# Kernel optimization log

Hardware: AMD Instinct MI355X
Metric: run time of the kernel (lower is better)

Reference implementation:

```python
import jax, jax.numpy as jnp
import numpy as np

H = 1024   # hidden_size
NH = 16    # num heads
DH = H // NH
L = 2      # attention levels
E = 8      # experts
F = 4 * H  # expert FFN hidden
B = 2
S = 1024
EPS = 1e-5
TOPK = 2
STD = 0.02


def setup_inputs() -> dict:
    key = jax.random.key(0)
    ks = jax.random.split(key, 12)
    def n(k, shp):
        return jax.random.normal(k, shp, jnp.float32) * STD
    return {
        "hidden_states": jax.random.normal(ks[0], (B, S, H), jnp.float32),
        "attention_mask": jnp.ones((B, S), jnp.int32),
        "ln1_g": jnp.ones((H,), jnp.float32), "ln1_b": jnp.zeros((H,), jnp.float32),
        "ln2_g": jnp.ones((H,), jnp.float32), "ln2_b": jnp.zeros((H,), jnp.float32),
        "Wq": n(ks[1], (L, H, H)), "Wk": n(ks[2], (L, H, H)),
        "Wv": n(ks[3], (L, H, H)), "Wo": n(ks[4], (L, H, H)),
        "bq": jnp.zeros((L, H), jnp.float32), "bk": jnp.zeros((L, H), jnp.float32),
        "bv": jnp.zeros((L, H), jnp.float32), "bo": jnp.zeros((L, H), jnp.float32),
        "level_logits": n(ks[5], (L,)),
        "Wr": n(ks[6], (H, E)), "br": jnp.zeros((E,), jnp.float32),
        "W1": n(ks[7], (E, H, F)), "b1": jnp.zeros((E, F), jnp.float32),
        "W2": n(ks[8], (E, F, H)), "b2": jnp.zeros((E, H), jnp.float32),
    }


def _ln(x, g, b):
    m = x.mean(-1, keepdims=True)
    v = x.var(-1, keepdims=True)
    return (x - m) * jax.lax.rsqrt(v + EPS) * g + b


def _mla(x, mask_f, Wq, Wk, Wv, Wo, bq, bk, bv, bo, level_logits):
    # Multi-level attention: one MHA per level, softmax-combined over levels.
    b_, s_, _ = x.shape
    def proj(W, bias):
        y = jnp.einsum('bsh,lhd->lbsd', x, W) + bias[:, None, None, :]
        return y.reshape(L, b_, s_, NH, DH)
    q, k, v = proj(Wq, bq), proj(Wk, bk), proj(Wv, bv)
    scores = jnp.einsum('lbqnd,lbknd->lbnqk', q, k) / np.float32(np.sqrt(DH))
    bias = (1.0 - mask_f)[None, :, None, None, :] * jnp.float32(-1e9)  # key-side mask
    attn = jax.nn.softmax(scores + bias, axis=-1)
    ctx = jnp.einsum('lbnqk,lbknd->lbqnd', attn, v).reshape(L, b_, s_, H)
    out = jnp.einsum('lbsh,lhd->lbsd', ctx, Wo) + bo[:, None, None, :]
    w = jax.nn.softmax(level_logits)
    return jnp.einsum('l,lbsd->bsd', w, out)


def _moe(x, Wr, br, W1, b1, W2, b2):
    # Top-2 softmax router with renormalized gates; dense expert compute,
    # sparse combine (math-equivalent to dispatch/combine without dropping).
    logits = x @ Wr + br                                  # [B,S,E]
    probs = jax.nn.softmax(logits, axis=-1)
    topv, topi = jax.lax.top_k(probs, TOPK)               # [B,S,K]
    gates = topv / topv.sum(-1, keepdims=True)
    combine = jnp.sum(jax.nn.one_hot(topi, E, dtype=x.dtype) * gates[..., None], axis=-2)  # [B,S,E]
    h = jax.nn.gelu(jnp.einsum('bsh,ehf->besf', x, W1) + b1[None, :, None, :])
    y = jnp.einsum('besf,efh->besh', h, W2) + b2[None, :, None, :]
    return jnp.einsum('bse,besh->bsh', combine, y), logits


def reference(hidden_states, attention_mask, ln1_g, ln1_b, ln2_g, ln2_b,
              Wq, Wk, Wv, Wo, bq, bk, bv, bo, level_logits,
              Wr, br, W1, b1, W2, b2):
    mask_f = attention_mask.astype(jnp.float32)
    attn = _mla(_ln(hidden_states, ln1_g, ln1_b), mask_f,
                Wq, Wk, Wv, Wo, bq, bk, bv, bo, level_logits)
    x = hidden_states + attn                  # residual 1 (dropout in eval = identity)
    moe_out, _router_logits = _moe(_ln(x, ln2_g, ln2_b), Wr, br, W1, b1, W2, b2)
    return x + moe_out                        # residual 2
```

## Files before the change

kernel.cpp:

```cpp
#include <hip/hip_runtime.h>
#include <hip/hip_bf16.h>
#include <stdint.h>

#define Hn   1024
#define NHn  16
#define DHn  64
#define Ln   2
#define En   8
#define Fn   4096
#define Bn   2
#define Sn   1024
#define Tn   2048
#define An   4096
#define KSPLIT 4

typedef __bf16 bf16_t;
typedef __bf16 bf16x2 __attribute__((ext_vector_type(2)));
typedef __bf16 bf16x4 __attribute__((ext_vector_type(4)));
typedef __bf16 bf16x8 __attribute__((ext_vector_type(8)));
typedef float  f32x4  __attribute__((ext_vector_type(4)));

__device__ __forceinline__ f32x4 mfma16(bf16x8 a, bf16x8 b, f32x4 c){
  return __builtin_amdgcn_mfma_f32_16x16x32_bf16(a, b, c, 0, 0, 0);
}
__device__ __forceinline__ void gload16(const void* gsrc, void* ldst){
  __builtin_amdgcn_global_load_lds((const __attribute__((address_space(1))) void*)gsrc,
                                   (__attribute__((address_space(3))) void*)ldst, 16, 0, 0);
}
__device__ __forceinline__ float gelu_f(float x){
  float u = 0.7978845608028654f * (x + 0.044715f * x * x * x);
  return 0.5f * x * (1.0f + tanhf(u));
}

__global__ __launch_bounds__(256)
void tcvt_k(const float* __restrict__ src, bf16_t* __restrict__ dst, int R, int C){
  __shared__ float tile[32][33];
  size_t moff = (size_t)blockIdx.z * R * C;
  src += moff; dst += moff;
  int c0 = blockIdx.x * 32, r0 = blockIdx.y * 32;
  int tx = threadIdx.x & 31, ty = threadIdx.x >> 5;
  #pragma unroll
  for (int i = 0; i < 32; i += 8)
    tile[ty + i][tx] = src[(size_t)(r0 + ty + i) * C + (c0 + tx)];
  __syncthreads();
  #pragma unroll
  for (int i = 0; i < 32; i += 8)
    dst[(size_t)(c0 + ty + i) * R + (r0 + tx)] = (bf16_t)tile[tx][ty + i];
}

__global__ __launch_bounds__(256)
void ln_k(const float* __restrict__ x, const float* __restrict__ gam,
          const float* __restrict__ bet, bf16_t* __restrict__ out){
  int row = blockIdx.x;
  const float4* xr = (const float4*)(x + (size_t)row * Hn);
  int t = threadIdx.x, lane = t & 63, w = t >> 6;
  float4 v = xr[t];
  float s  = v.x + v.y + v.z + v.w;
  float ss = v.x*v.x + v.y*v.y + v.z*v.z + v.w*v.w;
  #pragma unroll
  for (int mk = 1; mk < 64; mk <<= 1){ s += __shfl_xor(s, mk); ss += __shfl_xor(ss, mk); }
  __shared__ float r1[4], r2[4];
  if (lane == 0){ r1[w] = s; r2[w] = ss; }
  __syncthreads();
  float S1 = r1[0]+r1[1]+r1[2]+r1[3];
  float S2 = r2[0]+r2[1]+r2[2]+r2[3];
  float mean = S1 * (1.0f/Hn);
  float var  = S2 * (1.0f/Hn) - mean*mean;
  float rstd = rsqrtf(var + 1e-5f);
  int c = t * 4;
  bf16_t* o = out + (size_t)row * Hn + c;
  o[0] = (bf16_t)((v.x-mean)*rstd*gam[c+0] + bet[c+0]);
  o[1] = (bf16_t)((v.y-mean)*rstd*gam[c+1] + bet[c+1]);
  o[2] = (bf16_t)((v.z-mean)*rstd*gam[c+2] + bet[c+2]);
  o[3] = (bf16_t)((v.w-mean)*rstd*gam[c+3] + bet[c+3]);
}

__global__ __launch_bounds__(256)
void res_ln2_k(const float* __restrict__ x, const float* __restrict__ o0,
               const float* __restrict__ o1, const float* __restrict__ lvl,
               const float* __restrict__ gam, const float* __restrict__ bet,
               float* __restrict__ x2, bf16_t* __restrict__ xn2){
  int row = blockIdx.x, t = threadIdx.x, lane = t & 63, w = t >> 6;
  float l0 = lvl[0], l1 = lvl[1];
  float mx = fmaxf(l0, l1);
  float e0 = __expf(l0 - mx), e1 = __expf(l1 - mx);
  float inv = 1.f / (e0 + e1);
  float w0 = e0 * inv, w1 = e1 * inv;
  size_t base = (size_t)row * Hn;
  float4 xv = ((const float4*)(x  + base))[t];
  float4 a0 = ((const float4*)(o0 + base))[t];
  float4 a1 = ((const float4*)(o1 + base))[t];
  float4 v;
  v.x = xv.x + w0*a0.x + w1*a1.x;
  v.y = xv.y + w0*a0.y + w1*a1.y;
  v.z = xv.z + w0*a0.z + w1*a1.z;
  v.w = xv.w + w0*a0.w + w1*a1.w;
  ((float4*)(x2 + base))[t] = v;
  float s  = v.x + v.y + v.z + v.w;
  float ss = v.x*v.x + v.y*v.y + v.z*v.z + v.w*v.w;
  #pragma unroll
  for (int mk = 1; mk < 64; mk <<= 1){ s += __shfl_xor(s, mk); ss += __shfl_xor(ss, mk); }
  __shared__ float r1[4], r2[4];
  if (lane == 0){ r1[w] = s; r2[w] = ss; }
  __syncthreads();
  float S1 = r1[0]+r1[1]+r1[2]+r1[3];
  float S2 = r2[0]+r2[1]+r2[2]+r2[3];
  float mean = S1 * (1.0f/Hn);
  float var  = S2 * (1.0f/Hn) - mean*mean;
  float rstd = rsqrtf(var + 1e-5f);
  int c = t * 4;
  bf16_t* o = xn2 + base + c;
  o[0] = (bf16_t)((v.x-mean)*rstd*gam[c+0] + bet[c+0]);
  o[1] = (bf16_t)((v.y-mean)*rstd*gam[c+1] + bet[c+1]);
  o[2] = (bf16_t)((v.z-mean)*rstd*gam[c+2] + bet[c+2]);
  o[3] = (bf16_t)((v.w-mean)*rstd*gam[c+3] + bet[c+3]);
}

struct GP {
  const bf16_t* A;
  const bf16_t* Bt;
  const float*  bias;
  float*        fout;
  bf16_t*       bfout;
  const int*    list;
  const int*    counts;
  int Kstride;
  int Kloc;
};

template<int MODE>
__global__ __launch_bounds__(256)
void gemm_k(GP p){
  const int nt = blockIdx.x, mt = blockIdx.y, z = blockIdx.z;
  const bf16_t* A = p.A;
  const bf16_t* Bt = p.Bt;
  const float* bias = p.bias;
  const int* list = nullptr;
  int cnt = 0x7fffffff;
  int kbase = 0;
  if constexpr (MODE == 0){
    Bt += (size_t)z*Hn*Hn; bias += z*Hn;
  } else if constexpr (MODE == 1){
    Bt += (size_t)z*Hn*Hn; bias += z*Hn; A += (size_t)z*Bn*Sn*Hn;
  } else if constexpr (MODE == 3){
    cnt = p.counts[z];
    if (mt * 128 >= cnt) return;
    list = p.list + z * Tn;
    Bt += (size_t)z*Fn*Hn; bias += z*Fn;
  } else {
    int e = z >> 2;
    cnt = p.counts[e];
    if (mt * 128 >= cnt) return;
    list = p.list + e * Tn;
    Bt += (size_t)e*Hn*Fn; bias += e*Hn;
    kbase = (z & 3) * (Fn / KSPLIT);
  }
  const int Ks = p.Kstride;
  const int NT = p.Kloc >> 5;

  __shared__ bf16_t As[2][128*32];
  __shared__ bf16_t Bs[2][128*32];
  const int tid = threadIdx.x, lane = tid & 63, w = tid >> 6;
  const int wr = (w >> 1) * 64, wc = (w & 1) * 64;
  const int lane15 = lane & 15, kg = lane >> 4;

  const bf16_t* aptr[2];
  const bf16_t* bptr[2];
  int chunks[2];
  #pragma unroll
  for (int i = 0; i < 2; ++i){
    int ch = w*64 + lane + i*256;
    chunks[i] = ch;
    int row = ch >> 2, kc = (ch & 3) * 8;
    int ar;
    if constexpr (MODE == 3){ int g = mt*128 + row; if (g >= cnt) g = cnt - 1; ar = list[g] >> 1; }
    else if constexpr (MODE == 4){ int g = mt*128 + row; if (g >= cnt) g = cnt - 1; ar = list[g]; }
    else ar = mt*128 + row;
    aptr[i] = A  + (size_t)ar * Ks + kbase + kc;
    bptr[i] = Bt + (size_t)(nt*128 + row) * Ks + kbase + kc;
  }

  const f32x4 fz = {0.f,0.f,0.f,0.f};
  f32x4 acc[4][4];
  #pragma unroll
  for (int m = 0; m < 4; ++m)
    #pragma unroll
    for (int n = 0; n < 4; ++n) acc[m][n] = fz;

  #pragma unroll
  for (int i = 0; i < 2; ++i){
    gload16(aptr[i], &As[0][chunks[i]*8]);
    gload16(bptr[i], &Bs[0][chunks[i]*8]);
  }
  __syncthreads();

  int cur = 0;
  for (int t = 0; t < NT; ++t){
    if (t + 1 < NT){
      int k1 = (t+1) * 32;
      #pragma unroll
      for (int i = 0; i < 2; ++i){
        gload16(aptr[i] + k1, &As[cur^1][chunks[i]*8]);
        gload16(bptr[i] + k1, &Bs[cur^1][chunks[i]*8]);
      }
    }
    bf16x8 af[4], bfr[4];
    #pragma unroll
    for (int m = 0; m < 4; ++m) af[m]  = *(const bf16x8*)(&As[cur][(wr + m*16 + lane15)*32 + kg*8]);
    #pragma unroll
    for (int n = 0; n < 4; ++n) bfr[n] = *(const bf16x8*)(&Bs[cur][(wc + n*16 + lane15)*32 + kg*8]);
    #pragma unroll
    for (int m = 0; m < 4; ++m)
      #pragma unroll
      for (int n = 0; n < 4; ++n)
        acc[m][n] = mfma16(af[m], bfr[n], acc[m][n]);
    __syncthreads();
    cur ^= 1;
  }

  if constexpr (MODE == 0){
    bf16_t* outp = p.bfout + (size_t)z * (Bn*NHn*Sn*DHn);
    if (z < 4){
      #pragma unroll
      for (int m = 0; m < 4; ++m){
        int row0 = mt*128 + wr + m*16 + kg*4;
        #pragma unroll
        for (int n = 0; n < 4; ++n){
          int col = nt*128 + wc + n*16 + lane15;
          int nh = col >> 6, dh = col & 63;
          float bv = bias[col];
          f32x4 v = acc[m][n];
          #pragma unroll
          for (int r = 0; r < 4; ++r){
            int tk = row0 + r;
            int bb = tk >> 10, s = tk & 1023;
            outp[((size_t)(bb*NHn + nh)*Sn + s)*DHn + dh] = (bf16_t)(v[r] + bv);
          }
        }
      }
    } else {
      #pragma unroll
      for (int m = 0; m < 4; ++m){
        int row0 = mt*128 + wr + m*16 + kg*4;
        int bb = row0 >> 10, s = row0 & 1023;
        #pragma unroll
        for (int n = 0; n < 4; ++n){
          int col = nt*128 + wc + n*16 + lane15;
          int nh = col >> 6, dh = col & 63;
          float bv = bias[col];
          f32x4 v = acc[m][n];
          bf16x4 pk;
          pk[0] = (bf16_t)(v[0] + bv);
          pk[1] = (bf16_t)(v[1] + bv);
          pk[2] = (bf16_t)(v[2] + bv);
          pk[3] = (bf16_t)(v[3] + bv);
          *(bf16x4*)(outp + ((size_t)(bb*NHn + nh)*DHn + dh)*Sn + s) = pk;
        }
      }
    }
  } else if constexpr (MODE == 1){
    float* outp = p.fout + (size_t)z * Tn * Hn;
    #pragma unroll
    for (int m = 0; m < 4; ++m){
      int row0 = mt*128 + wr + m*16 + kg*4;
      #pragma unroll
      for (int n = 0; n < 4; ++n){
        int col = nt*128 + wc + n*16 + lane15;
        float bv = bias[col];
        f32x4 v = acc[m][n];
        #pragma unroll
        for (int r = 0; r < 4; ++r)
          outp[(size_t)(row0 + r)*Hn + col] = v[r] + bv;
      }
    }
  } else if constexpr (MODE == 3){
    #pragma unroll
    for (int m = 0; m < 4; ++m){
      int row0 = mt*128 + wr + m*16 + kg*4;
      #pragma unroll
      for (int n = 0; n < 4; ++n){
        int col = nt*128 + wc + n*16 + lane15;
        float bv = bias[col];
        f32x4 v = acc[m][n];
        #pragma unroll
        for (int r = 0; r < 4; ++r){
          int g = row0 + r;
          if (g < cnt){
            int aid = list[g];
            p.bfout[(size_t)aid*Fn + col] = (bf16_t)gelu_f(v[r] + bv);
          }
        }
      }
    }
  } else {
    float* outp = p.fout + (size_t)(z & 3) * An * Hn;
    bool addb = (z & 3) == 0;
    #pragma unroll
    for (int m = 0; m < 4; ++m){
      int row0 = mt*128 + wr + m*16 + kg*4;
      #pragma unroll
      for (int n = 0; n < 4; ++n){
        int col = nt*128 + wc + n*16 + lane15;
        float bv = addb ? bias[col] : 0.f;
        f32x4 v = acc[m][n];
        #pragma unroll
        for (int r = 0; r < 4; ++r){
          int g = row0 + r;
          if (g < cnt){
            int aid = list[g];
            outp[(size_t)aid*Hn + col] = v[r] + bv;
          }
        }
      }
    }
  }
}

__global__ __launch_bounds__(256)
void attn_k(const bf16_t* __restrict__ qh, const bf16_t* __restrict__ kh,
            const bf16_t* __restrict__ vtb, const int* __restrict__ amask,
            bf16_t* __restrict__ ctxb){
  int z  = blockIdx.x;
  int qb = blockIdx.y;
  int lvl = z >> 5, bb = (z >> 4) & 1, nh = z & 15;
  int tid = threadIdx.x, lane = tid & 63, w = tid >> 6;
  int lane15 = lane & 15, kg = lane >> 4;
  const bf16_t* Q  = qh  + (size_t)z * Sn * DHn;
  const bf16_t* Kp = kh  + (size_t)z * Sn * DHn;
  const bf16_t* Vt = vtb + (size_t)z * DHn * Sn;
  const int* mrow = amask + bb * Sn;
  __shared__ bf16_t Ks[2][32*64];
  __shared__ bf16_t Vs[2][64*32];
  __shared__ float bias_lds[Sn];
  __shared__ bf16_t p_lds[4][16*40];
  {
    int4 mv = ((const int4*)mrow)[tid];
    float4 bv;
    bv.x = mv.x ? 0.f : -1e9f;
    bv.y = mv.y ? 0.f : -1e9f;
    bv.z = mv.z ? 0.f : -1e9f;
    bv.w = mv.w ? 0.f : -1e9f;
    ((float4*)bias_lds)[tid] = bv;
  }
  int krow = w*8 + (lane >> 3);
  const bf16_t* ksrc = Kp + (size_t)krow*DHn + (((lane&7) ^ (krow&7)) << 3);
  int vrow = w*16 + (lane >> 2);
  const bf16_t* vsrc = Vt + (size_t)vrow*Sn + ((((lane&3) ^ ((vrow>>2)&3))) << 3);
  bf16_t* kdst[2] = { &Ks[0][w*512 + lane*8], &Ks[1][w*512 + lane*8] };
  bf16_t* vdst[2] = { &Vs[0][w*512 + lane*8], &Vs[1][w*512 + lane*8] };

  const f32x4 fz = {0.f,0.f,0.f,0.f};
  int qt = qb*4 + w;
  int qr = qt*16 + lane15;
  bf16x8 qa0 = *(const bf16x8*)(Q + (size_t)qr*DHn + kg*8);
  bf16x8 qa1 = *(const bf16x8*)(Q + (size_t)qr*DHn + 32 + kg*8);
  f32x4 ctxa[4] = {fz, fz, fz, fz};
  float m_ln = -1e30f;
  float s_ln = 0.f;
  float m_out[4] = {-1e30f,-1e30f,-1e30f,-1e30f};

  const int kslot0 = (kg ^ (lane15 & 7));
  const int kslot1 = ((kg + 4) ^ (lane15 & 7));
  const int ka_off0 = lane15*64 + kslot0*8;
  const int ka_off1 = lane15*64 + kslot1*8;
  const int kb_off0 = (16 + lane15)*64 + kslot0*8;
  const int kb_off1 = (16 + lane15)*64 + kslot1*8;

  gload16(ksrc, kdst[0]);
  gload16(vsrc, vdst[0]);
  __syncthreads();

  for (int kc = 0; kc < 32; ++kc){
    const int cur = kc & 1;
    const bf16_t* Kb = Ks[cur];
    const bf16_t* Vb = Vs[cur];
    if (kc + 1 < 32){
      gload16(ksrc + (size_t)(kc+1)*32*DHn, kdst[cur^1]);
      gload16(vsrc + (kc+1)*32,             vdst[cur^1]);
    }
    int k0 = kc * 32;
    bf16x8 ka0 = *(const bf16x8*)(Kb + ka_off0);
    bf16x8 ka1 = *(const bf16x8*)(Kb + ka_off1);
    bf16x8 kb0 = *(const bf16x8*)(Kb + kb_off0);
    bf16x8 kb1 = *(const bf16x8*)(Kb + kb_off1);
    f32x4 sA = mfma16(ka1, qa1, mfma16(ka0, qa0, fz));
    f32x4 sB = mfma16(kb1, qa1, mfma16(kb0, qa0, fz));
    float4 biasA = *(const float4*)(bias_lds + k0 + kg*4);
    float4 biasB = *(const float4*)(bias_lds + k0 + 16 + kg*4);
    float sv[8];
    sv[0] = sA[0]*0.125f + biasA.x;
    sv[1] = sA[1]*0.125f + biasA.y;
    sv[2] = sA[2]*0.125f + biasA.z;
    sv[3] = sA[3]*0.125f + biasA.w;
    sv[4] = sB[0]*0.125f + biasB.x;
    sv[5] = sB[1]*0.125f + biasB.y;
    sv[6] = sB[2]*0.125f + biasB.z;
    sv[7] = sB[3]*0.125f + biasB.w;
    float mx = fmaxf(fmaxf(fmaxf(sv[0],sv[1]),fmaxf(sv[2],sv[3])),
                     fmaxf(fmaxf(sv[4],sv[5]),fmaxf(sv[6],sv[7])));
    mx = fmaxf(mx, __shfl_xor(mx, 16));
    mx = fmaxf(mx, __shfl_xor(mx, 32));
    if (!__all(mx <= m_ln)){
      float mnew = fmaxf(m_ln, mx);
      s_ln *= __expf(m_ln - mnew);
      #pragma unroll
      for (int r = 0; r < 4; ++r){
        float mo = __shfl(mnew, kg*4 + r);
        float corr = __expf(m_out[r] - mo);
        ctxa[0][r] *= corr; ctxa[1][r] *= corr; ctxa[2][r] *= corr; ctxa[3][r] *= corr;
        m_out[r] = mo;
      }
      m_ln = mnew;
    }
    float pv[8];
    #pragma unroll
    for (int j = 0; j < 8; ++j){ pv[j] = __expf(sv[j] - m_ln); s_ln += pv[j]; }
    bf16_t* pr = p_lds[w] + lane15*40;
    *(bf16x2*)(pr + kg*4)          = (bf16x2){(bf16_t)pv[0], (bf16_t)pv[1]};
    *(bf16x2*)(pr + kg*4 + 2)      = (bf16x2){(bf16_t)pv[2], (bf16_t)pv[3]};
    *(bf16x2*)(pr + 16 + kg*4)     = (bf16x2){(bf16_t)pv[4], (bf16_t)pv[5]};
    *(bf16x2*)(pr + 16 + kg*4 + 2) = (bf16x2){(bf16_t)pv[6], (bf16_t)pv[7]};
    bf16x8 paf = *(const bf16x8*)(p_lds[w] + lane15*40 + kg*8);
    #pragma unroll
    for (int df = 0; df < 4; ++df){
      int r = df*16 + lane15;
      bf16x8 vbf = *(const bf16x8*)(Vb + r*32 + ((kg ^ ((r>>2)&3)) << 3));
      ctxa[df] = mfma16(paf, vbf, ctxa[df]);
    }
    __syncthreads();
  }
  s_ln += __shfl_xor(s_ln, 16);
  s_ln += __shfl_xor(s_ln, 32);
  #pragma unroll
  for (int r = 0; r < 4; ++r){
    float inv = 1.f / __shfl(s_ln, kg*4 + r);
    int srow = qt*16 + kg*4 + r;
    #pragma unroll
    for (int df = 0; df < 4; ++df){
      int d = df*16 + lane15;
      ctxb[((size_t)(lvl*2 + bb)*Sn + srow)*Hn + nh*DHn + d] = (bf16_t)(ctxa[df][r] * inv);
    }
  }
}

__global__ __launch_bounds__(64)
void router_k(const float* __restrict__ x2, const float* __restrict__ gam,
              const float* __restrict__ bet, const float* __restrict__ Wr,
              const float* __restrict__ br, float* __restrict__ gates,
              int* __restrict__ lists, int* __restrict__ counts){
  int t = blockIdx.x, lane = threadIdx.x;
  const float4* xr = (const float4*)(x2 + (size_t)t * Hn);
  float4 vbuf[4];
  float s = 0.f, ss = 0.f;
  #pragma unroll
  for (int i = 0; i < 4; ++i){
    float4 v = xr[lane + i*64];
    vbuf[i] = v;
    s  += v.x + v.y + v.z + v.w;
    ss += v.x*v.x + v.y*v.y + v.z*v.z + v.w*v.w;
  }
  #pragma unroll
  for (int mk = 1; mk < 64; mk <<= 1){ s += __shfl_xor(s, mk); ss += __shfl_xor(ss, mk); }
  float mean = s * (1.0f/Hn);
  float var  = ss * (1.0f/Hn) - mean*mean;
  float rstd = rsqrtf(var + 1e-5f);
  float a[8] = {0,0,0,0,0,0,0,0};
  #pragma unroll
  for (int i = 0; i < 4; ++i){
    int c = (lane + i*64) * 4;
    float4 v = vbuf[i];
    float xn[4] = {
      (v.x-mean)*rstd*gam[c+0] + bet[c+0],
      (v.y-mean)*rstd*gam[c+1] + bet[c+1],
      (v.z-mean)*rstd*gam[c+2] + bet[c+2],
      (v.w-mean)*rstd*gam[c+3] + bet[c+3]};
    #pragma unroll
    for (int j = 0; j < 4; ++j){
      const float* w = Wr + (size_t)(c + j) * En;
      #pragma unroll
      for (int e8 = 0; e8 < 8; ++e8) a[e8] += xn[j] * w[e8];
    }
  }
  #pragma unroll
  for (int e8 = 0; e8 < 8; ++e8)
    #pragma unroll
    for (int mk = 1; mk < 64; mk <<= 1) a[e8] += __shfl_xor(a[e8], mk);
  if (lane == 0){
    float lg[8]; float mx = -1e30f;
    #pragma unroll
    for (int e8 = 0; e8 < 8; ++e8){ lg[e8] = a[e8] + br[e8]; mx = fmaxf(mx, lg[e8]); }
    float p[8];
    #pragma unroll
    for (int e8 = 0; e8 < 8; ++e8) p[e8] = __expf(lg[e8] - mx);
    int i0 = 0; float v0 = p[0];
    #pragma unroll
    for (int e8 = 1; e8 < 8; ++e8) if (p[e8] > v0){ v0 = p[e8]; i0 = e8; }
    int i1 = -1; float v1 = -1.f;
    #pragma unroll
    for (int e8 = 0; e8 < 8; ++e8) if (e8 != i0 && p[e8] > v1){ v1 = p[e8]; i1 = e8; }
    float g0 = v0 / (v0 + v1), g1 = v1 / (v0 + v1);
    gates[2*t] = g0; gates[2*t+1] = g1;
    int s0 = atomicAdd(&counts[i0], 1); lists[i0*Tn + s0] = 2*t;
    int s1 = atomicAdd(&counts[i1], 1); lists[i1*Tn + s1] = 2*t + 1;
  }
}

__global__ __launch_bounds__(256)
void comb_k(const float* __restrict__ x2, const float* __restrict__ P,
            const float* __restrict__ gates, float* __restrict__ out){
  int t = blockIdx.x, i = threadIdx.x;
  float g0 = gates[2*t], g1 = gates[2*t+1];
  const size_t PS = (size_t)An * Hn;
  f32x4 s0 = {0,0,0,0}, s1 = {0,0,0,0};
  #pragma unroll
  for (int ks = 0; ks < KSPLIT; ++ks){
    f32x4 u0 = ((const f32x4*)(P + ks*PS + (size_t)(2*t)*Hn))[i];
    f32x4 u1 = ((const f32x4*)(P + ks*PS + (size_t)(2*t+1)*Hn))[i];
    s0 += u0; s1 += u1;
  }
  f32x4 va = ((const f32x4*)(x2 + (size_t)t*Hn))[i];
  f32x4 o = va + g0*s0 + g1*s1;
  ((f32x4*)(out + (size_t)t*Hn))[i] = o;
}

extern "C" void kernel_launch(void* const* d_in, const int* in_sizes, int n_in,
                              void* d_out, int out_size, void* d_ws, size_t ws_size,
                              hipStream_t stream)
{
  const float* x    = (const float*)d_in[0];
  const int* amask  = (const int*)d_in[1];
  const float* ln1g = (const float*)d_in[2];
  const float* ln1b = (const float*)d_in[3];
  const float* ln2g = (const float*)d_in[4];
  const float* ln2b = (const float*)d_in[5];
  const float* Wq   = (const float*)d_in[6];
  const float* Wk   = (const float*)d_in[7];
  const float* Wv   = (const float*)d_in[8];
  const float* Wo   = (const float*)d_in[9];
  const float* bq   = (const float*)d_in[10];
  const float* bk   = (const float*)d_in[11];
  const float* bv   = (const float*)d_in[12];
  const float* bo   = (const float*)d_in[13];
  const float* lvl  = (const float*)d_in[14];
  const float* Wr   = (const float*)d_in[15];
  const float* br   = (const float*)d_in[16];
  const float* W1   = (const float*)d_in[17];
  const float* b1   = (const float*)d_in[18];
  const float* W2   = (const float*)d_in[19];
  const float* b2   = (const float*)d_in[20];
  float* out = (float*)d_out;
  (void)in_sizes; (void)n_in; (void)out_size; (void)ws_size;

  char* wsp = (char*)d_ws;
  auto nxt = [&](size_t bytes) -> char* {
    char* r = wsp; wsp += (bytes + 255) & ~(size_t)255; return r;
  };
  bf16_t* wqkvT = (bf16_t*)nxt((size_t)6*Hn*Hn*2);
  bf16_t* woT   = (bf16_t*)nxt((size_t)Ln*Hn*Hn*2);
  bf16_t* w1t   = (bf16_t*)nxt((size_t)En*Fn*Hn*2);
  bf16_t* w2t   = (bf16_t*)nxt((size_t)En*Hn*Fn*2);
  float*  bqkv  = (float*)nxt((size_t)6*Hn*4);
  bf16_t* xn1   = (bf16_t*)nxt((size_t)Tn*Hn*2);
  bf16_t* qkvh  = (bf16_t*)nxt((size_t)6*Bn*NHn*Sn*DHn*2);
  bf16_t* ctxb  = (bf16_t*)nxt((size_t)Ln*Bn*Sn*Hn*2);
  float*  otmp  = (float*)nxt((size_t)Ln*Tn*Hn*4);
  float*  x2    = (float*)nxt((size_t)Tn*Hn*4);
  bf16_t* xn2   = (bf16_t*)nxt((size_t)Tn*Hn*2);
  float*  gates = (float*)nxt((size_t)Tn*2*4);
  int*    lists = (int*)nxt((size_t)En*Tn*4);
  int*    counts= (int*)nxt(256);
  bf16_t* hbuf  = (bf16_t*)nxt((size_t)An*Fn*2);
  float*  ybuf  = (float*)nxt((size_t)KSPLIT*An*Hn*4);

  hipMemsetAsync(counts, 0, En*sizeof(int), stream);
  hipMemcpyAsync(bqkv,          bq, (size_t)Ln*Hn*4, hipMemcpyDeviceToDevice, stream);
  hipMemcpyAsync(bqkv + 2*Hn,   bk, (size_t)Ln*Hn*4, hipMemcpyDeviceToDevice, stream);
  hipMemcpyAsync(bqkv + 4*Hn,   bv, (size_t)Ln*Hn*4, hipMemcpyDeviceToDevice, stream);

  tcvt_k<<<dim3(32,32,Ln), 256, 0, stream>>>(Wq, wqkvT,            Hn, Hn);
  tcvt_k<<<dim3(32,32,Ln), 256, 0, stream>>>(Wk, wqkvT + 2*Hn*Hn,  Hn, Hn);
  tcvt_k<<<dim3(32,32,Ln), 256, 0, stream>>>(Wv, wqkvT + 4*Hn*Hn,  Hn, Hn);
  tcvt_k<<<dim3(32,32,Ln), 256, 0, stream>>>(Wo, woT,              Hn, Hn);
  tcvt_k<<<dim3(Fn/32, Hn/32, En), 256, 0, stream>>>(W1, w1t, Hn, Fn);
  tcvt_k<<<dim3(Hn/32, Fn/32, En), 256, 0, stream>>>(W2, w2t, Fn, Hn);

  ln_k<<<Tn, 256, 0, stream>>>(x, ln1g, ln1b, xn1);

  { GP g{};
    g.A = xn1; g.Bt = wqkvT; g.bias = bqkv; g.bfout = qkvh;
    g.Kstride = Hn; g.Kloc = Hn;
    gemm_k<0><<<dim3(8,16,6), 256, 0, stream>>>(g); }

  {
    const bf16_t* qh = qkvh;
    const bf16_t* kh = qkvh + (size_t)2*Bn*NHn*Sn*DHn;
    const bf16_t* vt = qkvh + (size_t)4*Bn*NHn*Sn*DHn;
    attn_k<<<dim3(Ln*Bn*NHn, Sn/64), 256, 0, stream>>>(qh, kh, vt, amask, ctxb);
  }

  { GP g{};
    g.A = ctxb; g.Bt = woT; g.bias = bo; g.fout = otmp;
    g.Kstride = Hn; g.Kloc = Hn;
    gemm_k<1><<<dim3(8,16,2), 256, 0, stream>>>(g); }

  res_ln2_k<<<Tn, 256, 0, stream>>>(x, otmp, otmp + (size_t)Tn*Hn, lvl,
                                    ln2g, ln2b, x2, xn2);
  router_k<<<Tn, 64, 0, stream>>>(x2, ln2g, ln2b, Wr, br, gates, lists, counts);

  { GP g{};
    g.A = xn2; g.Bt = w1t; g.bias = b1; g.bfout = hbuf;
    g.list = lists; g.counts = counts;
    g.Kstride = Hn; g.Kloc = Hn;
    gemm_k<3><<<dim3(Fn/128, 16, En), 256, 0, stream>>>(g); }
  { GP g{};
    g.A = hbuf; g.Bt = w2t; g.bias = b2; g.fout = ybuf;
    g.list = lists; g.counts = counts;
    g.Kstride = Fn; g.Kloc = Fn / KSPLIT;
    gemm_k<4><<<dim3(Hn/128, 16, En*KSPLIT), 256, 0, stream>>>(g); }

  comb_k<<<Tn, 256, 0, stream>>>(x2, ybuf, gates, out);
}
```

Baseline: 489.2 us.

## Use 64-row tiles for expert GEMMs and store split-K partials in bf16

After: 509.5 us. +4.2%, slower.

```diff
diff --git a/kernel.cpp b/kernel.cpp
--- a/kernel.cpp
+++ b/kernel.cpp
@@ -131,6 +131,10 @@
 template<int MODE>
 __global__ __launch_bounds__(256)
 void gemm_k(GP p){
+  constexpr int BM  = (MODE == 3 || MODE == 4) ? 64 : 128;
+  constexpr int ACH = BM / 64;
+  constexpr int WRT = BM / 2;
+  constexpr int Mf  = WRT / 16;
   const int nt = blockIdx.x, mt = blockIdx.y, z = blockIdx.z;
   const bf16_t* A = p.A;
   const bf16_t* Bt = p.Bt;
@@ -144,13 +148,13 @@
     Bt += (size_t)z*Hn*Hn; bias += z*Hn; A += (size_t)z*Bn*Sn*Hn;
   } else if constexpr (MODE == 3){
     cnt = p.counts[z];
-    if (mt * 128 >= cnt) return;
+    if (mt * BM >= cnt) return;
     list = p.list + z * Tn;
     Bt += (size_t)z*Fn*Hn; bias += z*Fn;
   } else {
     int e = z >> 2;
     cnt = p.counts[e];
-    if (mt * 128 >= cnt) return;
+    if (mt * BM >= cnt) return;
     list = p.list + e * Tn;
     Bt += (size_t)e*Hn*Fn; bias += e*Hn;
     kbase = (z & 3) * (Fn / KSPLIT);
@@ -158,40 +162,46 @@
   const int Ks = p.Kstride;
   const int NT = p.Kloc >> 5;
 
-  __shared__ bf16_t As[2][128*32];
+  __shared__ bf16_t As[2][BM*32];
   __shared__ bf16_t Bs[2][128*32];
   const int tid = threadIdx.x, lane = tid & 63, w = tid >> 6;
-  const int wr = (w >> 1) * 64, wc = (w & 1) * 64;
+  const int wr = (w >> 1) * WRT, wc = (w & 1) * 64;
   const int lane15 = lane & 15, kg = lane >> 4;
 
-  const bf16_t* aptr[2];
-  const bf16_t* bptr[2];
-  int chunks[2];
-  #pragma unroll
-  for (int i = 0; i < 2; ++i){
-    int ch = w*64 + lane + i*256;
-    chunks[i] = ch;
+  const bf16_t* aptr[ACH];
+  int achk[ACH];
+  #pragma unroll
+  for (int i = 0; i < ACH; ++i){
+    int ch = tid + i*256;
+    achk[i] = ch;
     int row = ch >> 2, kc = (ch & 3) * 8;
     int ar;
-    if constexpr (MODE == 3){ int g = mt*128 + row; if (g >= cnt) g = cnt - 1; ar = list[g] >> 1; }
-    else if constexpr (MODE == 4){ int g = mt*128 + row; if (g >= cnt) g = cnt - 1; ar = list[g]; }
-    else ar = mt*128 + row;
-    aptr[i] = A  + (size_t)ar * Ks + kbase + kc;
+    if constexpr (MODE == 3){ int g = mt*BM + row; if (g >= cnt) g = cnt - 1; ar = list[g] >> 1; }
+    else if constexpr (MODE == 4){ int g = mt*BM + row; if (g >= cnt) g = cnt - 1; ar = list[g]; }
+    else ar = mt*BM + row;
+    aptr[i] = A + (size_t)ar * Ks + kbase + kc;
+  }
+  const bf16_t* bptr[2];
+  int bchk[2];
+  #pragma unroll
+  for (int i = 0; i < 2; ++i){
+    int ch = tid + i*256;
+    bchk[i] = ch;
+    int row = ch >> 2, kc = (ch & 3) * 8;
     bptr[i] = Bt + (size_t)(nt*128 + row) * Ks + kbase + kc;
   }
 
   const f32x4 fz = {0.f,0.f,0.f,0.f};
-  f32x4 acc[4][4];
-  #pragma unroll
-  for (int m = 0; m < 4; ++m)
+  f32x4 acc[Mf][4];
+  #pragma unroll
+  for (int m = 0; m < Mf; ++m)
     #pragma unroll
     for (int n = 0; n < 4; ++n) acc[m][n] = fz;
 
   #pragma unroll
-  for (int i = 0; i < 2; ++i){
-    gload16(aptr[i], &As[0][chunks[i]*8]);
-    gload16(bptr[i], &Bs[0][chunks[i]*8]);
-  }
+  for (int i = 0; i < ACH; ++i) gload16(aptr[i], &As[0][achk[i]*8]);
+  #pragma unroll
+  for (int i = 0; i < 2; ++i)   gload16(bptr[i], &Bs[0][bchk[i]*8]);
   __syncthreads();
 
   int cur = 0;
@@ -199,18 +209,17 @@
     if (t + 1 < NT){
       int k1 = (t+1) * 32;
       #pragma unroll
-      for (int i = 0; i < 2; ++i){
-        gload16(aptr[i] + k1, &As[cur^1][chunks[i]*8]);
-        gload16(bptr[i] + k1, &Bs[cur^1][chunks[i]*8]);
-      }
-    }
-    bf16x8 af[4], bfr[4];
-    #pragma unroll
-    for (int m = 0; m < 4; ++m) af[m]  = *(const bf16x8*)(&As[cur][(wr + m*16 + lane15)*32 + kg*8]);
-    #pragma unroll
-    for (int n = 0; n < 4; ++n) bfr[n] = *(const bf16x8*)(&Bs[cur][(wc + n*16 + lane15)*32 + kg*8]);
-    #pragma unroll
-    for (int m = 0; m < 4; ++m)
+      for (int i = 0; i < ACH; ++i) gload16(aptr[i] + k1, &As[cur^1][achk[i]*8]);
+      #pragma unroll
+      for (int i = 0; i < 2; ++i)   gload16(bptr[i] + k1, &Bs[cur^1][bchk[i]*8]);
+    }
+    bf16x8 af[Mf], bfr[4];
+    #pragma unroll
+    for (int m = 0; m < Mf; ++m) af[m]  = *(const bf16x8*)(&As[cur][(wr + m*16 + lane15)*32 + kg*8]);
+    #pragma unroll
+    for (int n = 0; n < 4; ++n)  bfr[n] = *(const bf16x8*)(&Bs[cur][(wc + n*16 + lane15)*32 + kg*8]);
+    #pragma unroll
+    for (int m = 0; m < Mf; ++m)
       #pragma unroll
       for (int n = 0; n < 4; ++n)
         acc[m][n] = mfma16(af[m], bfr[n], acc[m][n]);
@@ -222,8 +231,8 @@
     bf16_t* outp = p.bfout + (size_t)z * (Bn*NHn*Sn*DHn);
     if (z < 4){
       #pragma unroll
-      for (int m = 0; m < 4; ++m){
-        int row0 = mt*128 + wr + m*16 + kg*4;
+      for (int m = 0; m < Mf; ++m){
+        int row0 = mt*BM + wr + m*16 + kg*4;
         #pragma unroll
         for (int n = 0; n < 4; ++n){
           int col = nt*128 + wc + n*16 + lane15;
@@ -240,8 +249,8 @@
       }
     } else {
       #pragma unroll
-      for (int m = 0; m < 4; ++m){
-        int row0 = mt*128 + wr + m*16 + kg*4;
+      for (int m = 0; m < Mf; ++m){
+        int row0 = mt*BM + wr + m*16 + kg*4;
         int bb = row0 >> 10, s = row0 & 1023;
         #pragma unroll
         for (int n = 0; n < 4; ++n){
@@ -261,8 +270,8 @@
   } else if constexpr (MODE == 1){
     float* outp = p.fout + (size_t)z * Tn * Hn;
     #pragma unroll
-    for (int m = 0; m < 4; ++m){
-      int row0 = mt*128 + wr + m*16 + kg*4;
+    for (int m = 0; m < Mf; ++m){
+      int row0 = mt*BM + wr + m*16 + kg*4;
       #pragma unroll
       for (int n = 0; n < 4; ++n){
         int col = nt*128 + wc + n*16 + lane15;
@@ -275,8 +284,8 @@
     }
   } else if constexpr (MODE == 3){
     #pragma unroll
-    for (int m = 0; m < 4; ++m){
-      int row0 = mt*128 + wr + m*16 + kg*4;
+    for (int m = 0; m < Mf; ++m){
+      int row0 = mt*BM + wr + m*16 + kg*4;
       #pragma unroll
       for (int n = 0; n < 4; ++n){
         int col = nt*128 + wc + n*16 + lane15;
@@ -293,11 +302,11 @@
       }
     }
   } else {
-    float* outp = p.fout + (size_t)(z & 3) * An * Hn;
+    bf16_t* outp = p.bfout + (size_t)(z & 3) * An * Hn;
     bool addb = (z & 3) == 0;
     #pragma unroll
-    for (int m = 0; m < 4; ++m){
-      int row0 = mt*128 + wr + m*16 + kg*4;
+    for (int m = 0; m < Mf; ++m){
+      int row0 = mt*BM + wr + m*16 + kg*4;
       #pragma unroll
       for (int n = 0; n < 4; ++n){
         int col = nt*128 + wc + n*16 + lane15;
@@ -308,7 +317,7 @@
           int g = row0 + r;
           if (g < cnt){
             int aid = list[g];
-            outp[(size_t)aid*Hn + col] = v[r] + bv;
+            outp[(size_t)aid*Hn + col] = (bf16_t)(v[r] + bv);
           }
         }
       }
@@ -506,7 +515,7 @@
 }
 
 __global__ __launch_bounds__(256)
-void comb_k(const float* __restrict__ x2, const float* __restrict__ P,
+void comb_k(const float* __restrict__ x2, const bf16_t* __restrict__ P,
             const float* __restrict__ gates, float* __restrict__ out){
   int t = blockIdx.x, i = threadIdx.x;
   float g0 = gates[2*t], g1 = gates[2*t+1];
@@ -514,9 +523,10 @@
   f32x4 s0 = {0,0,0,0}, s1 = {0,0,0,0};
   #pragma unroll
   for (int ks = 0; ks < KSPLIT; ++ks){
-    f32x4 u0 = ((const f32x4*)(P + ks*PS + (size_t)(2*t)*Hn))[i];
-    f32x4 u1 = ((const f32x4*)(P + ks*PS + (size_t)(2*t+1)*Hn))[i];
-    s0 += u0; s1 += u1;
+    bf16x4 u0 = *(const bf16x4*)(P + ks*PS + (size_t)(2*t)*Hn + i*4);
+    bf16x4 u1 = *(const bf16x4*)(P + ks*PS + (size_t)(2*t+1)*Hn + i*4);
+    #pragma unroll
+    for (int j = 0; j < 4; ++j){ s0[j] += (float)u0[j]; s1[j] += (float)u1[j]; }
   }
   f32x4 va = ((const f32x4*)(x2 + (size_t)t*Hn))[i];
   f32x4 o = va + g0*s0 + g1*s1;
@@ -570,7 +580,7 @@
   int*    lists = (int*)nxt((size_t)En*Tn*4);
   int*    counts= (int*)nxt(256);
   bf16_t* hbuf  = (bf16_t*)nxt((size_t)An*Fn*2);
-  float*  ybuf  = (float*)nxt((size_t)KSPLIT*An*Hn*4);
+  bf16_t* ybuf  = (bf16_t*)nxt((size_t)KSPLIT*An*Hn*2);
 
   hipMemsetAsync(counts, 0, En*sizeof(int), stream);
   hipMemcpyAsync(bqkv,          bq, (size_t)Ln*Hn*4, hipMemcpyDeviceToDevice, stream);
@@ -611,12 +621,12 @@
     g.A = xn2; g.Bt = w1t; g.bias = b1; g.bfout = hbuf;
     g.list = lists; g.counts = counts;
     g.Kstride = Hn; g.Kloc = Hn;
-    gemm_k<3><<<dim3(Fn/128, 16, En), 256, 0, stream>>>(g); }
+    gemm_k<3><<<dim3(Fn/128, Tn/64, En), 256, 0, stream>>>(g); }
   { GP g{};
-    g.A = hbuf; g.Bt = w2t; g.bias = b2; g.fout = ybuf;
+    g.A = hbuf; g.Bt = w2t; g.bfout = ybuf; g.bias = b2;
     g.list = lists; g.counts = counts;
     g.Kstride = Fn; g.Kloc = Fn / KSPLIT;
-    gemm_k<4><<<dim3(Hn/128, 16, En*KSPLIT), 256, 0, stream>>>(g); }
+    gemm_k<4><<<dim3(Hn/128, Tn/64, En*KSPLIT), 256, 0, stream>>>(g); }
 
   comb_k<<<Tn, 256, 0, stream>>>(x2, ybuf, gates, out);
 }
```
